# Kernel tuning notes

Measured on AMD Instinct MI355X. Metric: run time of the kernel, lower is better.

Reference implementation:

```python
import jax, jax.numpy as jnp
import numpy as np

HIDDEN = 1024
HEADS = 16
HEAD_DIM = HIDDEN // HEADS
FF = 4 * HIDDEN
B, S = 2, 2048


def _linear_params(key, out_dim, in_dim):
    kw, kb = jax.random.split(key)
    bound = 1.0 / np.sqrt(in_dim)
    W = jax.random.uniform(kw, (out_dim, in_dim), jnp.float32, -bound, bound)
    b = jax.random.uniform(kb, (out_dim,), jnp.float32, -bound, bound)
    return W, b


def setup_inputs() -> dict:
    key = jax.random.key(0)
    ks = jax.random.split(key, 8)
    x = jax.random.normal(ks[0], (B, S, HIDDEN), jnp.float32)
    attention_mask = jnp.ones((B, S), jnp.float32)
    Wq, bq = _linear_params(ks[1], HIDDEN, HIDDEN)
    Wk, bk = _linear_params(ks[2], HIDDEN, HIDDEN)
    Wv, bv = _linear_params(ks[3], HIDDEN, HIDDEN)
    Wo, bo = _linear_params(ks[4], HIDDEN, HIDDEN)
    W1, b1 = _linear_params(ks[5], FF, HIDDEN)
    W2, b2 = _linear_params(ks[6], HIDDEN, FF)
    g1 = jnp.ones((HIDDEN,), jnp.float32); be1 = jnp.zeros((HIDDEN,), jnp.float32)
    g2 = jnp.ones((HIDDEN,), jnp.float32); be2 = jnp.zeros((HIDDEN,), jnp.float32)
    return dict(x=x, attention_mask=attention_mask,
                Wq=Wq, bq=bq, Wk=Wk, bk=bk, Wv=Wv, bv=bv, Wo=Wo, bo=bo,
                W1=W1, b1=b1, W2=W2, b2=b2,
                g1=g1, be1=be1, g2=g2, be2=be2)


def _layer_norm(x, g, b, eps=1e-5):
    mu = jnp.mean(x, axis=-1, keepdims=True)
    var = jnp.mean(jnp.square(x - mu), axis=-1, keepdims=True)
    return (x - mu) * jax.lax.rsqrt(var + eps) * g + b


def reference(x, attention_mask, Wq, bq, Wk, bk, Wv, bv, Wo, bo,
              W1, b1, W2, b2, g1, be1, g2, be2):
    # Dropout is identity (eval mode / deterministic reference).
    residual = x
    h = _layer_norm(x, g1, be1)
    # [B,S,H] -> [B,nH,S,dh]
    def heads(t):
        return t.reshape(B, S, HEADS, HEAD_DIM).transpose(0, 2, 1, 3)
    q = heads(h @ Wq.T + bq)
    k = heads(h @ Wk.T + bk)
    v = heads(h @ Wv.T + bv)
    scores = jnp.einsum('bhqd,bhkd->bhqk', q, k) / np.sqrt(HEAD_DIM).astype(np.float32)
    scores = scores + (attention_mask[:, None, None, :] - 1.0) * 10000.0
    attn = jax.nn.softmax(scores, axis=-1)
    ctx = jnp.einsum('bhqk,bhkd->bhqd', attn, v)
    ctx = ctx.transpose(0, 2, 1, 3).reshape(B, S, HIDDEN)
    attn_out = ctx @ Wo.T + bo
    x = residual + attn_out
    residual = x
    h = _layer_norm(x, g2, be2)
    h = jax.nn.gelu(h @ W1.T + b1, approximate=False)
    h = h @ W2.T + b2
    return residual + h
```

## Files before the change

### kernel.cpp

```cpp
#include <hip/hip_runtime.h>
#include <hip/hip_bf16.h>
#include <math.h>

typedef __bf16 bf16;
typedef __bf16 bf16x4v __attribute__((ext_vector_type(4)));
typedef __bf16 bf16x8 __attribute__((ext_vector_type(8)));
typedef float  f32x4  __attribute__((ext_vector_type(4)));

#define HIDDEN 1024
#define TOKENS 4096
#define FFDIM  4096
#define SEQ    2048
#define NHEAD  16

#define LOG2E 1.44269504088896340736f

__device__ __forceinline__ void async_copy16(bf16* lds, const bf16* g)
{
    __builtin_amdgcn_global_load_lds(
        (__attribute__((address_space(1))) void*)g,
        (__attribute__((address_space(3))) void*)lds,
        16, 0, 0);
}

__global__ __launch_bounds__(256) void cvt_kernel(const float* __restrict__ in,
                                                  bf16* __restrict__ out, int n)
{
    int i = (blockIdx.x * 256 + threadIdx.x) * 4;
    if (i >= n) return;
    float4 v = *(const float4*)&in[i];
    bf16x4v o = { (bf16)v.x, (bf16)v.y, (bf16)v.z, (bf16)v.w };
    *(bf16x4v*)&out[i] = o;
}

__global__ __launch_bounds__(256) void cvt4_kernel(const float* __restrict__ s0,
    const float* __restrict__ s1, const float* __restrict__ s2, const float* __restrict__ s3,
    bf16* __restrict__ out)
{
    const int M1 = 1 << 20;
    int i = (blockIdx.x * 256 + threadIdx.x) * 4;
    int sel = i >> 20;
    const float* src = (sel == 0) ? s0 : (sel == 1) ? s1 : (sel == 2) ? s2 : s3;
    float4 v = *(const float4*)&src[i & (M1 - 1)];
    bf16x4v o = { (bf16)v.x, (bf16)v.y, (bf16)v.z, (bf16)v.w };
    *(bf16x4v*)&out[i] = o;
}

__global__ __launch_bounds__(256) void concat_bias_kernel(const float* __restrict__ bq,
    const float* __restrict__ bk, const float* __restrict__ bv, float* __restrict__ o)
{
    int i = blockIdx.x * 256 + threadIdx.x;
    float v = (i < 1024) ? bq[i] : (i < 2048 ? bk[i - 1024] : bv[i - 2048]);
    o[i] = v;
}

__global__ __launch_bounds__(256) void ln_kernel(const float* __restrict__ in,
    const float* __restrict__ g, const float* __restrict__ be, bf16* __restrict__ out)
{
    int row = blockIdx.x;
    int tid = threadIdx.x;
    const float* x = in + (size_t)row * HIDDEN;
    int i0 = tid * 4;
    float4 v = *(const float4*)&x[i0];
    float s  = v.x + v.y + v.z + v.w;
    float s2 = v.x*v.x + v.y*v.y + v.z*v.z + v.w*v.w;
    #pragma unroll
    for (int off = 32; off > 0; off >>= 1) { s += __shfl_xor(s, off); s2 += __shfl_xor(s2, off); }
    __shared__ float red[2][4];
    int wave = tid >> 6;
    if ((tid & 63) == 0) { red[0][wave] = s; red[1][wave] = s2; }
    __syncthreads();
    float ts  = red[0][0] + red[0][1] + red[0][2] + red[0][3];
    float ts2 = red[1][0] + red[1][1] + red[1][2] + red[1][3];
    float mu   = ts  * (1.0f / HIDDEN);
    float var  = ts2 * (1.0f / HIDDEN) - mu * mu;
    float rstd = rsqrtf(var + 1e-5f);
    float4 gg = *(const float4*)&g[i0];
    float4 bb = *(const float4*)&be[i0];
    bf16x4v o;
    o[0] = (bf16)((v.x - mu) * rstd * gg.x + bb.x);
    o[1] = (bf16)((v.y - mu) * rstd * gg.y + bb.y);
    o[2] = (bf16)((v.z - mu) * rstd * gg.z + bb.z);
    o[3] = (bf16)((v.w - mu) * rstd * gg.w + bb.w);
    *(bf16x4v*)&out[(size_t)row * HIDDEN + i0] = o;
}

template<int BM, int EPI, typename OT>
__global__ __launch_bounds__(256) void gemm_bt(const bf16* __restrict__ A, const bf16* __restrict__ Bt,
    const float* __restrict__ bias, const float* __restrict__ res, OT* __restrict__ C,
    int M, int N, int K)
{
    constexpr int MT = BM / 32;
    __shared__ bf16 As[BM * 64];
    __shared__ bf16 Bs[128 * 64];
    int tid  = threadIdx.x;
    int wave = tid >> 6, lane = tid & 63;
    int lm = lane & 15, quad = lane >> 4;
    int m0 = blockIdx.x * BM, n0 = blockIdx.y * 128;
    int wm = (wave >> 1) * (MT * 16), wn = (wave & 1) * 64;
    int r8 = lane >> 3, c8 = lane & 7;
    int gsw = (c8 ^ (r8 & 7)) * 8;
    f32x4 acc[MT][4] = {};
    for (int k0 = 0; k0 < K; k0 += 64) {
        #pragma unroll
        for (int ch = wave; ch < BM / 8; ch += 4)
            async_copy16(As + ch * 512, &A[(size_t)(m0 + ch * 8 + r8) * K + k0 + gsw]);
        #pragma unroll
        for (int ch = wave; ch < 16; ch += 4)
            async_copy16(Bs + ch * 512, &Bt[(size_t)(n0 + ch * 8 + r8) * K + k0 + gsw]);
        __syncthreads();
        bf16x8 af[MT][2], bfr[4][2];
        #pragma unroll
        for (int ks = 0; ks < 2; ks++) {
            int co = ((ks * 4 + quad) ^ (lm & 7)) * 8;
            #pragma unroll
            for (int t = 0; t < MT; t++) af[t][ks]  = *(const bf16x8*)&As[(wm + t * 16 + lm) * 64 + co];
            #pragma unroll
            for (int t = 0; t < 4; t++)  bfr[t][ks] = *(const bf16x8*)&Bs[(wn + t * 16 + lm) * 64 + co];
        }
        #pragma unroll
        for (int mt = 0; mt < MT; mt++)
            #pragma unroll
            for (int nt = 0; nt < 4; nt++)
                #pragma unroll
                for (int ks = 0; ks < 2; ks++)
                    acc[mt][nt] = __builtin_amdgcn_mfma_f32_16x16x32_bf16(af[mt][ks], bfr[nt][ks], acc[mt][nt], 0, 0, 0);
        __syncthreads();
    }
    #pragma unroll
    for (int mt = 0; mt < MT; mt++) {
        #pragma unroll
        for (int nt = 0; nt < 4; nt++) {
            int col = n0 + wn + nt * 16 + lm;
            float bv = bias[col];
            #pragma unroll
            for (int r = 0; r < 4; r++) {
                int row = m0 + wm + mt * 16 + quad * 4 + r;
                float vv = acc[mt][nt][r] + bv;
                if (EPI == 1) vv = 0.5f * vv * (1.0f + erff(vv * 0.70710678118654752f));
                if (EPI == 2) vv += res[(size_t)row * N + col];
                C[(size_t)row * N + col] = (OT)vv;
            }
        }
    }
}

__global__ __launch_bounds__(256) void gemm_qkv(const bf16* __restrict__ A, const bf16* __restrict__ W,
    const float* __restrict__ bias, bf16* __restrict__ qb, bf16* __restrict__ kb, bf16* __restrict__ vt)
{
    constexpr int K = HIDDEN;
    __shared__ bf16 As[128 * 64];
    __shared__ bf16 Bs[128 * 64];
    int tid  = threadIdx.x;
    int wave = tid >> 6, lane = tid & 63;
    int lm = lane & 15, quad = lane >> 4;
    int m0 = blockIdx.x * 128, n0 = blockIdx.y * 128;
    int wm = (wave >> 1) * 64, wn = (wave & 1) * 64;
    int r8 = lane >> 3, c8 = lane & 7;
    int gsw = (c8 ^ (r8 & 7)) * 8;
    f32x4 acc[4][4] = {};
    for (int k0 = 0; k0 < K; k0 += 64) {
        #pragma unroll
        for (int ch = wave; ch < 16; ch += 4) {
            async_copy16(As + ch * 512, &A[(size_t)(m0 + ch * 8 + r8) * K + k0 + gsw]);
            async_copy16(Bs + ch * 512, &W[(size_t)(n0 + ch * 8 + r8) * K + k0 + gsw]);
        }
        __syncthreads();
        bf16x8 af[4][2], bfr[4][2];
        #pragma unroll
        for (int ks = 0; ks < 2; ks++) {
            int co = ((ks * 4 + quad) ^ (lm & 7)) * 8;
            #pragma unroll
            for (int t = 0; t < 4; t++) {
                af[t][ks]  = *(const bf16x8*)&As[(wm + t * 16 + lm) * 64 + co];
                bfr[t][ks] = *(const bf16x8*)&Bs[(wn + t * 16 + lm) * 64 + co];
            }
        }
        #pragma unroll
        for (int mt = 0; mt < 4; mt++)
            #pragma unroll
            for (int nt = 0; nt < 4; nt++)
                #pragma unroll
                for (int ks = 0; ks < 2; ks++)
                    acc[mt][nt] = __builtin_amdgcn_mfma_f32_16x16x32_bf16(af[mt][ks], bfr[nt][ks], acc[mt][nt], 0, 0, 0);
        __syncthreads();
    }
    int region = n0 >> 10;
    #pragma unroll
    for (int mt = 0; mt < 4; mt++) {
        #pragma unroll
        for (int nt = 0; nt < 4; nt++) {
            int col = n0 + wn + nt * 16 + lm;
            float bv = bias[col];
            int cl = col & 1023;
            #pragma unroll
            for (int r = 0; r < 4; r++) {
                int row = m0 + wm + mt * 16 + quad * 4 + r;
                float vv = acc[mt][nt][r] + bv;
                if (region == 0)      qb[(size_t)row * HIDDEN + cl] = (bf16)vv;
                else if (region == 1) kb[(size_t)row * HIDDEN + cl] = (bf16)vv;
                else {
                    int h = cl >> 6, d = cl & 63;
                    int b = row >> 11, s = row & 2047;
                    vt[(((size_t)(b * NHEAD + h)) * 64 + d) * SEQ + s] = (bf16)vv;
                }
            }
        }
    }
}

__global__ __launch_bounds__(512) void attn_kernel(const bf16* __restrict__ Q, const bf16* __restrict__ K,
    const bf16* __restrict__ Vt, const float* __restrict__ mask, bf16* __restrict__ O)
{
    __shared__ bf16 Ks[64 * 64];
    __shared__ bf16 Vs[64 * 64];
    __shared__ bf16 Ps[8][16 * 72];
    int tid = threadIdx.x, wave = tid >> 6, lane = tid & 63;
    int lm = lane & 15, quad = lane >> 4;
    int bh = blockIdx.y, b = bh >> 4, h = bh & 15;
    int q0 = blockIdx.x * 128 + wave * 16;
    const size_t base  = ((size_t)b * SEQ) * HIDDEN + h * 64;
    const size_t vbase = (size_t)bh * 64 * SEQ;
    int srow8 = lane >> 3, spos = lane & 7;
    bf16x8 qf[2];
    #pragma unroll
    for (int ks = 0; ks < 2; ks++)
        qf[ks] = *(const bf16x8*)&Q[base + (size_t)(q0 + lm) * HIDDEN + ks * 32 + quad * 8];
    bf16x8 onesf;
    #pragma unroll
    for (int i = 0; i < 8; i++) onesf[i] = (bf16)1.0f;
    f32x4 o[4] = {};
    f32x4 lacc = {};
    const float c0 = 0.125f * LOG2E;
    const float cmk = 10000.0f * LOG2E;
    const float coff = -(cmk + 16.0f);
    bf16* pw = &Ps[wave][0];
    for (int kt = 0; kt < SEQ; kt += 64) {
        __syncthreads();
        {
            int r = wave * 8 + srow8;
            int gc = spos ^ (r & 7);
            async_copy16(&Ks[wave * 512], &K [base  + (size_t)(kt + r) * HIDDEN + gc * 8]);
            async_copy16(&Vs[wave * 512], &Vt[vbase + (size_t)r * SEQ + kt + gc * 8]);
        }
        __syncthreads();
        f32x4 st[4] = {};
        #pragma unroll
        for (int nt = 0; nt < 4; nt++) {
            #pragma unroll
            for (int ks = 0; ks < 2; ks++) {
                bf16x8 kf = *(const bf16x8*)&Ks[(nt * 16 + lm) * 64 + (((ks * 4 + quad) ^ (lm & 7)) * 8)];
                st[nt] = __builtin_amdgcn_mfma_f32_16x16x32_bf16(kf, qf[ks], st[nt], 0, 0, 0);
            }
        }
        #pragma unroll
        for (int nt = 0; nt < 4; nt++) {
            float4 mv = *(const float4*)&mask[b * SEQ + kt + nt * 16 + quad * 4];
            float p0 = __builtin_amdgcn_exp2f(st[nt][0] * c0 + (mv.x * cmk + coff));
            float p1 = __builtin_amdgcn_exp2f(st[nt][1] * c0 + (mv.y * cmk + coff));
            float p2 = __builtin_amdgcn_exp2f(st[nt][2] * c0 + (mv.z * cmk + coff));
            float p3 = __builtin_amdgcn_exp2f(st[nt][3] * c0 + (mv.w * cmk + coff));
            bf16x4v pk = { (bf16)p0, (bf16)p1, (bf16)p2, (bf16)p3 };
            *(bf16x4v*)&pw[lm * 72 + nt * 16 + quad * 4] = pk;
        }
        bf16x8 pf[2];
        #pragma unroll
        for (int ks = 0; ks < 2; ks++)
            pf[ks] = *(const bf16x8*)&pw[lm * 72 + ks * 32 + quad * 8];
        lacc = __builtin_amdgcn_mfma_f32_16x16x32_bf16(pf[0], onesf, lacc, 0, 0, 0);
        lacc = __builtin_amdgcn_mfma_f32_16x16x32_bf16(pf[1], onesf, lacc, 0, 0, 0);
        #pragma unroll
        for (int dt = 0; dt < 4; dt++) {
            #pragma unroll
            for (int ks = 0; ks < 2; ks++) {
                bf16x8 vf = *(const bf16x8*)&Vs[(dt * 16 + lm) * 64 + (((ks * 4 + quad) ^ (lm & 7)) * 8)];
                o[dt] = __builtin_amdgcn_mfma_f32_16x16x32_bf16(pf[ks], vf, o[dt], 0, 0, 0);
            }
        }
    }
    #pragma unroll
    for (int r = 0; r < 4; r++) {
        float inv = 1.0f / lacc[r];
        #pragma unroll
        for (int dt = 0; dt < 4; dt++) {
            float val = o[dt][r] * inv;
            O[base + (size_t)(q0 + quad * 4 + r) * HIDDEN + dt * 16 + lm] = (bf16)val;
        }
    }
}

extern "C" void kernel_launch(void* const* d_in, const int* in_sizes, int n_in,
                              void* d_out, int out_size, void* d_ws, size_t ws_size,
                              hipStream_t stream)
{
    (void)in_sizes; (void)n_in; (void)out_size; (void)ws_size;
    const float* x    = (const float*)d_in[0];
    const float* mask = (const float*)d_in[1];
    const float* Wq   = (const float*)d_in[2];
    const float* bq   = (const float*)d_in[3];
    const float* Wk   = (const float*)d_in[4];
    const float* bk   = (const float*)d_in[5];
    const float* Wv   = (const float*)d_in[6];
    const float* bv   = (const float*)d_in[7];
    const float* Wo   = (const float*)d_in[8];
    const float* bo   = (const float*)d_in[9];
    const float* W1   = (const float*)d_in[10];
    const float* b1   = (const float*)d_in[11];
    const float* W2   = (const float*)d_in[12];
    const float* b2   = (const float*)d_in[13];
    const float* g1   = (const float*)d_in[14];
    const float* be1  = (const float*)d_in[15];
    const float* g2   = (const float*)d_in[16];
    const float* be2  = (const float*)d_in[17];
    float* out = (float*)d_out;

    const size_t M1 = 1024u * 1024u;
    bf16* ws    = (bf16*)d_ws;
    bf16* Wqkv_b = ws;
    bf16* Wo_b  = ws + 3 * M1;
    bf16* W1_b  = ws + 4 * M1;
    bf16* W2_b  = ws + 8 * M1;
    bf16* qb    = ws + 12 * M1;
    bf16* kb    = ws + 16 * M1;
    bf16* vt    = ws + 20 * M1;
    bf16* cx    = ws + 24 * M1;
    bf16* h     = ws + 28 * M1;
    bf16* ffb   = ws + 12 * M1;
    float* biasqkv = (float*)(ws + 24 * M1);

    cvt4_kernel<<<dim3(4096), 256, 0, stream>>>(Wq, Wk, Wv, Wo, Wqkv_b);
    cvt_kernel<<<dim3(4 * M1 / 1024), 256, 0, stream>>>(W1, W1_b, 4 * M1);
    cvt_kernel<<<dim3(4 * M1 / 1024), 256, 0, stream>>>(W2, W2_b, 4 * M1);
    concat_bias_kernel<<<dim3(12), 256, 0, stream>>>(bq, bk, bv, biasqkv);

    ln_kernel<<<dim3(TOKENS), 256, 0, stream>>>(x, g1, be1, h);
    gemm_qkv<<<dim3(32, 24), 256, 0, stream>>>(h, Wqkv_b, biasqkv, qb, kb, vt);
    attn_kernel<<<dim3(SEQ / 128, 32), 512, 0, stream>>>(qb, kb, vt, mask, cx);
    gemm_bt<64, 2, float><<<dim3(64, 8), 256, 0, stream>>>(cx, Wo_b, bo, x, out, TOKENS, HIDDEN, HIDDEN);
    ln_kernel<<<dim3(TOKENS), 256, 0, stream>>>(out, g2, be2, h);
    gemm_bt<128, 1, bf16><<<dim3(32, 32), 256, 0, stream>>>(h, W1_b, b1, nullptr, ffb, TOKENS, FFDIM, HIDDEN);
    gemm_bt<64, 2, float><<<dim3(64, 8), 256, 0, stream>>>(ffb, W2_b, b2, out, out, TOKENS, HIDDEN, FFDIM);
}
```

Before: 392.8 us.

## Double-buffer K/V tiles in attention and merge weight conversions into one kernel

Result: faster. 384.5 us (-2.1%).

```diff
diff --git a/kernel.cpp b/kernel.cpp
--- a/kernel.cpp
+++ b/kernel.cpp
@@ -23,25 +23,18 @@
         16, 0, 0);
 }
 
-__global__ __launch_bounds__(256) void cvt_kernel(const float* __restrict__ in,
-                                                  bf16* __restrict__ out, int n)
-{
-    int i = (blockIdx.x * 256 + threadIdx.x) * 4;
-    if (i >= n) return;
-    float4 v = *(const float4*)&in[i];
-    bf16x4v o = { (bf16)v.x, (bf16)v.y, (bf16)v.z, (bf16)v.w };
-    *(bf16x4v*)&out[i] = o;
-}
-
-__global__ __launch_bounds__(256) void cvt4_kernel(const float* __restrict__ s0,
-    const float* __restrict__ s1, const float* __restrict__ s2, const float* __restrict__ s3,
-    bf16* __restrict__ out)
-{
-    const int M1 = 1 << 20;
-    int i = (blockIdx.x * 256 + threadIdx.x) * 4;
-    int sel = i >> 20;
-    const float* src = (sel == 0) ? s0 : (sel == 1) ? s1 : (sel == 2) ? s2 : s3;
-    float4 v = *(const float4*)&src[i & (M1 - 1)];
+__global__ __launch_bounds__(256) void cvt_all_kernel(const float* __restrict__ wq,
+    const float* __restrict__ wk, const float* __restrict__ wv, const float* __restrict__ wo,
+    const float* __restrict__ w1, const float* __restrict__ w2, bf16* __restrict__ out)
+{
+    size_t i = ((size_t)blockIdx.x * 256 + threadIdx.x) * 4;
+    int sel = (int)(i >> 20);
+    const float* src;
+    size_t off;
+    if (sel < 4) { src = (sel == 0) ? wq : (sel == 1) ? wk : (sel == 2) ? wv : wo; off = i & ((1u << 20) - 1); }
+    else if (sel < 8) { src = w1; off = i - ((size_t)4 << 20); }
+    else              { src = w2; off = i - ((size_t)8 << 20); }
+    float4 v = *(const float4*)&src[off];
     bf16x4v o = { (bf16)v.x, (bf16)v.y, (bf16)v.z, (bf16)v.w };
     *(bf16x4v*)&out[i] = o;
 }
@@ -212,8 +205,8 @@
 __global__ __launch_bounds__(512) void attn_kernel(const bf16* __restrict__ Q, const bf16* __restrict__ K,
     const bf16* __restrict__ Vt, const float* __restrict__ mask, bf16* __restrict__ O)
 {
-    __shared__ bf16 Ks[64 * 64];
-    __shared__ bf16 Vs[64 * 64];
+    __shared__ bf16 Ks[2][64 * 64];
+    __shared__ bf16 Vs[2][64 * 64];
     __shared__ bf16 Ps[8][16 * 72];
     int tid = threadIdx.x, wave = tid >> 6, lane = tid & 63;
     int lm = lane & 15, quad = lane >> 4;
@@ -235,21 +228,25 @@
     const float cmk = 10000.0f * LOG2E;
     const float coff = -(cmk + 16.0f);
     bf16* pw = &Ps[wave][0];
-    for (int kt = 0; kt < SEQ; kt += 64) {
-        __syncthreads();
-        {
-            int r = wave * 8 + srow8;
-            int gc = spos ^ (r & 7);
-            async_copy16(&Ks[wave * 512], &K [base  + (size_t)(kt + r) * HIDDEN + gc * 8]);
-            async_copy16(&Vs[wave * 512], &Vt[vbase + (size_t)r * SEQ + kt + gc * 8]);
-        }
-        __syncthreads();
+    int r = wave * 8 + srow8;
+    int gc = spos ^ (r & 7);
+    auto stage = [&](int buf, int kt) {
+        async_copy16(&Ks[buf][wave * 512], &K [base  + (size_t)(kt + r) * HIDDEN + gc * 8]);
+        async_copy16(&Vs[buf][wave * 512], &Vt[vbase + (size_t)r * SEQ + kt + gc * 8]);
+    };
+    stage(0, 0);
+    for (int ti = 0; ti < SEQ / 64; ti++) {
+        __syncthreads();
+        if (ti + 1 < SEQ / 64) stage((ti + 1) & 1, (ti + 1) * 64);
+        const bf16* ksb = Ks[ti & 1];
+        const bf16* vsb = Vs[ti & 1];
+        int kt = ti * 64;
         f32x4 st[4] = {};
         #pragma unroll
         for (int nt = 0; nt < 4; nt++) {
             #pragma unroll
             for (int ks = 0; ks < 2; ks++) {
-                bf16x8 kf = *(const bf16x8*)&Ks[(nt * 16 + lm) * 64 + (((ks * 4 + quad) ^ (lm & 7)) * 8)];
+                bf16x8 kf = *(const bf16x8*)&ksb[(nt * 16 + lm) * 64 + (((ks * 4 + quad) ^ (lm & 7)) * 8)];
                 st[nt] = __builtin_amdgcn_mfma_f32_16x16x32_bf16(kf, qf[ks], st[nt], 0, 0, 0);
             }
         }
@@ -273,18 +270,18 @@
         for (int dt = 0; dt < 4; dt++) {
             #pragma unroll
             for (int ks = 0; ks < 2; ks++) {
-                bf16x8 vf = *(const bf16x8*)&Vs[(dt * 16 + lm) * 64 + (((ks * 4 + quad) ^ (lm & 7)) * 8)];
+                bf16x8 vf = *(const bf16x8*)&vsb[(dt * 16 + lm) * 64 + (((ks * 4 + quad) ^ (lm & 7)) * 8)];
                 o[dt] = __builtin_amdgcn_mfma_f32_16x16x32_bf16(pf[ks], vf, o[dt], 0, 0, 0);
             }
         }
     }
     #pragma unroll
-    for (int r = 0; r < 4; r++) {
-        float inv = 1.0f / lacc[r];
+    for (int rr = 0; rr < 4; rr++) {
+        float inv = 1.0f / lacc[rr];
         #pragma unroll
         for (int dt = 0; dt < 4; dt++) {
-            float val = o[dt][r] * inv;
-            O[base + (size_t)(q0 + quad * 4 + r) * HIDDEN + dt * 16 + lm] = (bf16)val;
+            float val = o[dt][rr] * inv;
+            O[base + (size_t)(q0 + quad * 4 + rr) * HIDDEN + dt * 16 + lm] = (bf16)val;
         }
     }
 }
@@ -328,9 +325,7 @@
     bf16* ffb   = ws + 12 * M1;
     float* biasqkv = (float*)(ws + 24 * M1);
 
-    cvt4_kernel<<<dim3(4096), 256, 0, stream>>>(Wq, Wk, Wv, Wo, Wqkv_b);
-    cvt_kernel<<<dim3(4 * M1 / 1024), 256, 0, stream>>>(W1, W1_b, 4 * M1);
-    cvt_kernel<<<dim3(4 * M1 / 1024), 256, 0, stream>>>(W2, W2_b, 4 * M1);
+    cvt_all_kernel<<<dim3(12288), 256, 0, stream>>>(Wq, Wk, Wv, Wo, W1, W2, Wqkv_b);
     concat_bias_kernel<<<dim3(12), 256, 0, stream>>>(bq, bk, bv, biasqkv);
 
     ln_kernel<<<dim3(TOKENS), 256, 0, stream>>>(x, g1, be1, h);
```
